# Optimization experiments

Measured on AMD Instinct MI355X. Metric: run time of the kernel, lower is better.

The kernel has to match this reference:

```python
import jax, jax.numpy as jnp
import numpy as np

N_C = 64
D = 128

def setup_inputs() -> dict:
    key = jax.random.key(0)
    embeddings = jax.random.normal(key, (1024, N_C * D), dtype=jnp.float32)
    return {"embeddings": embeddings}

def reference(embeddings) -> jnp.ndarray:
    two_b, _ = embeddings.shape
    B = two_b // 2
    # (2, B, n_c, d), softmax over last dim
    q = jax.nn.softmax(embeddings.reshape(2, B, N_C, D), axis=-1)
    q_a, q_b = q[0], q[1]  # (B, n_c, d)

    self_sim_loss = -(q_a * q_b).sum() / (B * N_C)

    q_a2 = q_a * q_a
    q_b2 = q_b * q_b
    # Faithful to the repeat/repeat_interleave + bmm: block (i, j) of the
    # (n_c^2, d, d) product equals q2[:, j].T @ q2[:, i]  -> einsum over batch.
    prod_a = jnp.einsum('bjc,bid->ijcd', q_a2, q_a2)  # (n_c, n_c, d, d)
    prod_b = jnp.einsum('bjc,bid->ijcd', q_b2, q_b2)

    # mask out diagonal cluster pairs i == j (done before sqrt in original;
    # entries are strictly positive so masking after sqrt is identical)
    offdiag = (~jnp.eye(N_C, dtype=bool))[:, :, None, None]  # (n_c, n_c, 1, 1)

    raw_a = jnp.where(offdiag, jnp.sqrt(prod_a), 0.0).sum()
    raw_b = jnp.where(offdiag, jnp.sqrt(prod_b), 0.0).sum()

    scale = (N_C * N_C - N_C) * (B ** 0.5)
    cluster_loss = -(raw_a / scale + raw_b / scale) / 2
    return self_sim_loss + cluster_loss
```

## Files before the change

kernel.cpp:

```cpp
#include <hip/hip_runtime.h>
#include <cstdint>
#include <cstddef>

#define NCLUS 64
#define DIM   128
#define BATCH 512
#define QCOLS 8192
#define NPAIR 2016
#define TSTRB (QCOLS * BATCH)
#define FP8SCALE 256.0f

typedef float f32x16 __attribute__((ext_vector_type(16)));
typedef int   i32x4  __attribute__((ext_vector_type(4)));
typedef int   i32x8  __attribute__((ext_vector_type(8)));


__device__ __forceinline__ void ld_lds16(const void* g, void* l) {
  __builtin_amdgcn_global_load_lds(
      (__attribute__((address_space(1))) void*)g,
      (__attribute__((address_space(3))) void*)l, 16, 0, 0);
}

#define VM4_BAR() asm volatile("s_waitcnt vmcnt(4)\n\ts_barrier" ::: "memory")
#define VM0_BAR() asm volatile("s_waitcnt vmcnt(0)\n\ts_barrier" ::: "memory")

__global__ __launch_bounds__(512) void softmax_q2_kernel(
    const float* __restrict__ emb, uint8_t* __restrict__ q2t,
    float* __restrict__ dotPart) {
  __shared__ uint32_t T32[2 * 64 * 33];
  __shared__ float red[8];
  const int c  = blockIdx.y;
  const int bq = blockIdx.x;
  const int tid = threadIdx.x;
  const int w = tid >> 6, lane = tid & 63;
  const int sub = lane >> 5;
  const int col = lane & 31;

  float4 qa = {0.f, 0.f, 0.f, 0.f};
  float dot = 0.f;

#pragma unroll
  for (int k = 0; k < 8; ++k) {
    const int t  = k & 1;
    const int bl = w * 8 + (k >> 1) * 2 + sub;
    const int b  = bq * 64 + bl;
    const float4 v = *(const float4*)(emb +
        ((size_t)(t * BATCH + b) * QCOLS + (size_t)c * DIM + col * 4));

    float mx = fmaxf(fmaxf(v.x, v.y), fmaxf(v.z, v.w));
#pragma unroll
    for (int off = 1; off < 32; off <<= 1) mx = fmaxf(mx, __shfl_xor(mx, off));
    float e0 = __expf(v.x - mx), e1 = __expf(v.y - mx);
    float e2 = __expf(v.z - mx), e3 = __expf(v.w - mx);
    float s = (e0 + e1) + (e2 + e3);
#pragma unroll
    for (int off = 1; off < 32; off <<= 1) s += __shfl_xor(s, off);
    const float inv = 1.0f / s;
    const float q0 = e0 * inv, q1 = e1 * inv, q2 = e2 * inv, q3 = e3 * inv;

    if (t == 0) { qa.x = q0; qa.y = q1; qa.z = q2; qa.w = q3; }
    else        { dot += qa.x * q0 + qa.y * q1 + qa.z * q2 + qa.w * q3; }

    int pk = __builtin_amdgcn_cvt_pk_fp8_f32(q0 * q0 * FP8SCALE,
                                             q1 * q1 * FP8SCALE, 0, false);
    pk = __builtin_amdgcn_cvt_pk_fp8_f32(q2 * q2 * FP8SCALE,
                                         q3 * q3 * FP8SCALE, pk, true);
    T32[(t * 64 + bl) * 33 + col] = (uint32_t)pk;
  }
  __syncthreads();

#pragma unroll
  for (int it = 0; it < 2; ++it) {
    int ch = it * 512 + tid;
    int t = ch >> 9, d = (ch >> 2) & 127, b16 = ch & 3;
    const int dq = d >> 2, sh = (d & 3) * 8;
    uint32_t w0 = 0, w1 = 0, w2 = 0, w3 = 0;
#pragma unroll
    for (int r = 0; r < 4; ++r) {
      w0 |= ((T32[(t * 64 + b16 * 16 +  0 + r) * 33 + dq] >> sh) & 0xFFu) << (8 * r);
      w1 |= ((T32[(t * 64 + b16 * 16 +  4 + r) * 33 + dq] >> sh) & 0xFFu) << (8 * r);
      w2 |= ((T32[(t * 64 + b16 * 16 +  8 + r) * 33 + dq] >> sh) & 0xFFu) << (8 * r);
      w3 |= ((T32[(t * 64 + b16 * 16 + 12 + r) * 33 + dq] >> sh) & 0xFFu) << (8 * r);
    }
    size_t off = (size_t)t * TSTRB + (size_t)(c * DIM + d) * BATCH +
                 (size_t)bq * 64 + b16 * 16;
    uint4 o; o.x = w0; o.y = w1; o.z = w2; o.w = w3;
    *(uint4*)(q2t + off) = o;
  }

#pragma unroll
  for (int off = 1; off < 64; off <<= 1) dot += __shfl_xor(dot, off);
  if (lane == 0) red[w] = dot;
  __syncthreads();
  if (tid == 0) {
    float dt = 0.f;
#pragma unroll
    for (int i = 0; i < 8; ++i) dt += red[i];
    dotPart[blockIdx.y * 8 + blockIdx.x] = dt;
  }
}

__global__ __launch_bounds__(256) void gram_sqrt_kernel(
    const uint8_t* __restrict__ q2t, float* __restrict__ Spart) {
  __shared__ uint8_t L[3 * 16384 + 16];

  int sidx = ((int)blockIdx.x & 7) * 252 + ((int)blockIdx.x >> 3);
  int q = sidx, gi = 0;
  while (q >= 64 * gi + 28) { q -= 64 * gi + 28; ++gi; }
  int I, J;
  if (q < 64 * gi) {
    int gj = q >> 6, r = q & 63;
    I = gi * 8 + (r >> 3);
    J = gj * 8 + (r & 7);
  } else {
    int dq = q - 64 * gi;
    int il = 1;
    while (il * (il + 1) / 2 <= dq) ++il;
    I = gi * 8 + il;
    J = gi * 8 + (dq - il * (il - 1) / 2);
  }

  const uint8_t* baseA = q2t + (size_t)J * (DIM * BATCH);
  const uint8_t* baseB = q2t + (size_t)I * (DIM * BATCH);

  const int tid  = threadIdx.x;
  const int lane = tid & 63, w = tid >> 6;
  const int wm = w & 1, wn = w >> 1;

  const int t0 = tid, t1 = 256 + tid;
  const int r0s = t0 >> 2, r1s = t1 >> 2;
  const int rot0 = (r0s + (r0s >> 2)) & 3;
  const int rot1 = (r1s + (r1s >> 2)) & 3;
  const int c0s = ((t0 & 3) - rot0) & 3;
  const int c1s = ((t1 & 3) - rot1) & 3;
  const size_t g0 = (size_t)r0s * BATCH + c0s * 16;
  const size_t g1 = (size_t)r1s * BATCH + c1s * 16;
  uint8_t* Lb = L;
  const int ldsw = w * 1024;

  const int h = lane >> 5, r31 = lane & 31;
  const int rot = (r31 + (r31 >> 2)) & 3;
  const int ro1 = ((2 * h + rot) & 3) * 16;
  const int ro2 = ((2 * h + 1 + rot) & 3) * 16;
  const int ArowO = (wm * 64 + r31) * 64;
  const int BrowO = 8192 + (wn * 64 + r31) * 64;

  f32x16 acc[2][2];
#pragma unroll
  for (int i = 0; i < 2; ++i)
#pragma unroll
    for (int j = 0; j < 2; ++j) acc[i][j] = (f32x16)(0.f);

  float S0 = 0.f, S1 = 0.f;

#define CHOFF64(i) ((size_t)((i) >> 3) * TSTRB + (size_t)((i) & 7) * 64)
#define STAGE(bufb, ck) do {                                       \
    ld_lds16(baseA + (ck) + g0, Lb + (bufb) + ldsw);               \
    ld_lds16(baseA + (ck) + g1, Lb + (bufb) + 4096 + ldsw);        \
    ld_lds16(baseB + (ck) + g0, Lb + (bufb) + 8192 + ldsw);        \
    ld_lds16(baseB + (ck) + g1, Lb + (bufb) + 12288 + ldsw);       \
  } while (0)
#define MFMA(a, b, c) __builtin_amdgcn_mfma_scale_f32_32x32x64_f8f6f4(        \
    (a), (b), (c), 0, 0, 0, 0x7F7F7F7F, 0, 0x7F7F7F7F)

  STAGE(0, CHOFF64(0));
  STAGE(16384, CHOFF64(1));

#pragma unroll
  for (int m = 0; m < 16; ++m) {
    if (m < 15) VM4_BAR(); else VM0_BAR();

    if (m < 14) STAGE(((m + 2) % 3) * 16384, CHOFF64(m + 2));

    const int be = (m % 3) * 16384;
    i32x4 alo[2], ahi[2], blo[2], bhi[2];
#pragma unroll
    for (int g = 0; g < 2; ++g) {
      alo[g] = *(const i32x4*)(Lb + be + ArowO + g * 2048 + ro1);
      ahi[g] = *(const i32x4*)(Lb + be + ArowO + g * 2048 + ro2);
      blo[g] = *(const i32x4*)(Lb + be + BrowO + g * 2048 + ro1);
      bhi[g] = *(const i32x4*)(Lb + be + BrowO + g * 2048 + ro2);
    }
    i32x8 af[2], bf[2];
#pragma unroll
    for (int g = 0; g < 2; ++g) {
      af[g] = (i32x8){alo[g].x, alo[g].y, alo[g].z, alo[g].w,
                      ahi[g].x, ahi[g].y, ahi[g].z, ahi[g].w};
      bf[g] = (i32x8){blo[g].x, blo[g].y, blo[g].z, blo[g].w,
                      bhi[g].x, bhi[g].y, bhi[g].z, bhi[g].w};
    }
    __builtin_amdgcn_s_setprio(1);
#pragma unroll
    for (int i = 0; i < 2; ++i)
#pragma unroll
      for (int j = 0; j < 2; ++j)
        acc[i][j] = MFMA(af[i], bf[j], acc[i][j]);
    __builtin_amdgcn_s_setprio(0);

    if (m == 7) {
#pragma unroll
      for (int i = 0; i < 2; ++i)
#pragma unroll
        for (int j = 0; j < 2; ++j) {
#pragma unroll
          for (int e = 0; e < 16; ++e) S0 += sqrtf(acc[i][j][e]);
          acc[i][j] = (f32x16)(0.f);
        }
    }
  }

#pragma unroll
  for (int i = 0; i < 2; ++i)
#pragma unroll
    for (int j = 0; j < 2; ++j)
#pragma unroll
      for (int e = 0; e < 16; ++e) S1 += sqrtf(acc[i][j][e]);

  float local = (S0 + S1) * (1.0f / 256.0f);
#pragma unroll
  for (int off = 1; off < 64; off <<= 1) local += __shfl_xor(local, off);
  float* fred = (float*)(L + 3 * 16384);
  if (lane == 0) fred[w] = local;
  __syncthreads();
  if (tid == 0) Spart[blockIdx.x] = fred[0] + fred[1] + fred[2] + fred[3];
}

__global__ __launch_bounds__(256) void finalize_kernel(
    const float* __restrict__ P, float* __restrict__ out) {
  __shared__ float rd[8];
  const int tid = threadIdx.x;
  float d = 0.f, s = 0.f;
  for (int i = tid; i < 512; i += 256) d += P[i];
  for (int i = tid; i < NPAIR; i += 256) s += P[512 + i];
#pragma unroll
  for (int off = 1; off < 64; off <<= 1) { d += __shfl_xor(d, off); s += __shfl_xor(s, off); }
  const int w = tid >> 6;
  if ((tid & 63) == 0) { rd[w] = d; rd[4 + w] = s; }
  __syncthreads();
  if (tid == 0) {
    float dt = rd[0] + rd[1] + rd[2] + rd[3];
    float st = rd[4] + rd[5] + rd[6] + rd[7];
    out[0] = -dt / 32768.0f - st / (4032.0f * 22.62741699796952f);
  }
}

extern "C" void kernel_launch(void* const* d_in, const int* in_sizes, int n_in,
                              void* d_out, int out_size, void* d_ws, size_t ws_size,
                              hipStream_t stream) {
  const float* emb = (const float*)d_in[0];
  float* out = (float*)d_out;
  float* P = (float*)d_ws;
  uint8_t* q2t = (uint8_t*)d_ws + 16384;

  softmax_q2_kernel<<<dim3(8, 64), 512, 0, stream>>>(emb, q2t, P);
  gram_sqrt_kernel<<<dim3(NPAIR), 256, 0, stream>>>(q2t, P + 512);
  finalize_kernel<<<1, 256, 0, stream>>>(P, out);
}
```

Baseline: 126.6 us.

## Tile gram kernel over 256x256 cluster-pair super-tiles with 512-thread blocks

Replaces the per-cluster-pair gram kernel (2016 blocks, 128x128 tiles) with a super-tile kernel in which each 512-thread block computes a 256x256 product covering two clusters by two clusters, giving 528 blocks over the lower triangle. Each loaded tile is reused across more MFMAs, which cuts global and LDS traffic per flop. On diagonal super-tiles only the warps holding the strictly off-diagonal cluster pair do MFMAs, so some warps idle there. The softmax kernel also drops to 256 threads per block, with each thread doing twice as many rows.

```diff
diff --git a/kernel.cpp b/kernel.cpp
--- a/kernel.cpp
+++ b/kernel.cpp
@@ -6,7 +6,7 @@
 #define DIM   128
 #define BATCH 512
 #define QCOLS 8192
-#define NPAIR 2016
+#define NSUPER 528
 #define TSTRB (QCOLS * BATCH)
 #define FP8SCALE 256.0f
 
@@ -24,11 +24,11 @@
 #define VM4_BAR() asm volatile("s_waitcnt vmcnt(4)\n\ts_barrier" ::: "memory")
 #define VM0_BAR() asm volatile("s_waitcnt vmcnt(0)\n\ts_barrier" ::: "memory")
 
-__global__ __launch_bounds__(512) void softmax_q2_kernel(
+__global__ __launch_bounds__(256) void softmax_q2_kernel(
     const float* __restrict__ emb, uint8_t* __restrict__ q2t,
     float* __restrict__ dotPart) {
   __shared__ uint32_t T32[2 * 64 * 33];
-  __shared__ float red[8];
+  __shared__ float red[4];
   const int c  = blockIdx.y;
   const int bq = blockIdx.x;
   const int tid = threadIdx.x;
@@ -40,9 +40,9 @@
   float dot = 0.f;
 
 #pragma unroll
-  for (int k = 0; k < 8; ++k) {
+  for (int k = 0; k < 16; ++k) {
     const int t  = k & 1;
-    const int bl = w * 8 + (k >> 1) * 2 + sub;
+    const int bl = w * 16 + (k >> 1) * 2 + sub;
     const int b  = bq * 64 + bl;
     const float4 v = *(const float4*)(emb +
         ((size_t)(t * BATCH + b) * QCOLS + (size_t)c * DIM + col * 4));
@@ -70,8 +70,8 @@
   __syncthreads();
 
 #pragma unroll
-  for (int it = 0; it < 2; ++it) {
-    int ch = it * 512 + tid;
+  for (int it = 0; it < 4; ++it) {
+    int ch = it * 256 + tid;
     int t = ch >> 9, d = (ch >> 2) & 127, b16 = ch & 3;
     const int dq = d >> 2, sh = (d & 3) * 8;
     uint32_t w0 = 0, w1 = 0, w2 = 0, w3 = 0;
@@ -92,49 +92,30 @@
   for (int off = 1; off < 64; off <<= 1) dot += __shfl_xor(dot, off);
   if (lane == 0) red[w] = dot;
   __syncthreads();
-  if (tid == 0) {
-    float dt = 0.f;
-#pragma unroll
-    for (int i = 0; i < 8; ++i) dt += red[i];
-    dotPart[blockIdx.y * 8 + blockIdx.x] = dt;
-  }
-}
-
-__global__ __launch_bounds__(256) void gram_sqrt_kernel(
+  if (tid == 0) dotPart[blockIdx.y * 8 + blockIdx.x] = red[0] + red[1] + red[2] + red[3];
+}
+
+__global__ __launch_bounds__(512, 2) void gram_super_kernel(
     const uint8_t* __restrict__ q2t, float* __restrict__ Spart) {
-  __shared__ uint8_t L[3 * 16384 + 16];
-
-  int sidx = ((int)blockIdx.x & 7) * 252 + ((int)blockIdx.x >> 3);
-  int q = sidx, gi = 0;
-  while (q >= 64 * gi + 28) { q -= 64 * gi + 28; ++gi; }
-  int I, J;
-  if (q < 64 * gi) {
-    int gj = q >> 6, r = q & 63;
-    I = gi * 8 + (r >> 3);
-    J = gj * 8 + (r & 7);
-  } else {
-    int dq = q - 64 * gi;
-    int il = 1;
-    while (il * (il + 1) / 2 <= dq) ++il;
-    I = gi * 8 + il;
-    J = gi * 8 + (dq - il * (il - 1) / 2);
-  }
-
-  const uint8_t* baseA = q2t + (size_t)J * (DIM * BATCH);
-  const uint8_t* baseB = q2t + (size_t)I * (DIM * BATCH);
+  __shared__ uint8_t L[3 * 32768 + 32];
+
+  int sidx = ((int)blockIdx.x & 7) * 66 + ((int)blockIdx.x >> 3);
+  int gi = 0;
+  while ((gi + 1) * (gi + 2) / 2 <= sidx) ++gi;
+  int gj = sidx - gi * (gi + 1) / 2;
+  const bool diag = (gi == gj);
+
+  const uint8_t* baseA = q2t + (size_t)gj * (256 * BATCH);
+  const uint8_t* baseB = q2t + (size_t)gi * (256 * BATCH);
 
   const int tid  = threadIdx.x;
   const int lane = tid & 63, w = tid >> 6;
   const int wm = w & 1, wn = w >> 1;
 
-  const int t0 = tid, t1 = 256 + tid;
-  const int r0s = t0 >> 2, r1s = t1 >> 2;
-  const int rot0 = (r0s + (r0s >> 2)) & 3;
-  const int rot1 = (r1s + (r1s >> 2)) & 3;
-  const int c0s = ((t0 & 3) - rot0) & 3;
-  const int c1s = ((t1 & 3) - rot1) & 3;
-  const size_t g0 = (size_t)r0s * BATCH + c0s * 16;
-  const size_t g1 = (size_t)r1s * BATCH + c1s * 16;
+  const int rs = tid >> 2;
+  const int rot_s = (rs + (rs >> 2)) & 3;
+  const int cs = ((tid & 3) - rot_s) & 3;
+  const size_t gsrc = (size_t)rs * BATCH + cs * 16;
   uint8_t* Lb = L;
   const int ldsw = w * 1024;
 
@@ -142,87 +123,100 @@
   const int rot = (r31 + (r31 >> 2)) & 3;
   const int ro1 = ((2 * h + rot) & 3) * 16;
   const int ro2 = ((2 * h + 1 + rot) & 3) * 16;
-  const int ArowO = (wm * 64 + r31) * 64;
-  const int BrowO = 8192 + (wn * 64 + r31) * 64;
-
-  f32x16 acc[2][2];
-#pragma unroll
-  for (int i = 0; i < 2; ++i)
+  const int ArO = (wm * 128 + r31) * 64;
+  const int BrO = 16384 + (wn * 64 + r31) * 64;
+
+  const bool take = !diag || (wm == 0 && wn >= 2);
+
+  f32x16 acc[4][2];
+#pragma unroll
+  for (int i = 0; i < 4; ++i)
 #pragma unroll
     for (int j = 0; j < 2; ++j) acc[i][j] = (f32x16)(0.f);
 
   float S0 = 0.f, S1 = 0.f;
 
 #define CHOFF64(i) ((size_t)((i) >> 3) * TSTRB + (size_t)((i) & 7) * 64)
-#define STAGE(bufb, ck) do {                                       \
-    ld_lds16(baseA + (ck) + g0, Lb + (bufb) + ldsw);               \
-    ld_lds16(baseA + (ck) + g1, Lb + (bufb) + 4096 + ldsw);        \
-    ld_lds16(baseB + (ck) + g0, Lb + (bufb) + 8192 + ldsw);        \
-    ld_lds16(baseB + (ck) + g1, Lb + (bufb) + 12288 + ldsw);       \
+#define STAGE(bufb, ck) do {                                           \
+    ld_lds16(baseA + (ck) + gsrc,         Lb + (bufb) + ldsw);         \
+    ld_lds16(baseA + (ck) + gsrc + 65536, Lb + (bufb) + 8192 + ldsw);  \
+    ld_lds16(baseB + (ck) + gsrc,         Lb + (bufb) + 16384 + ldsw); \
+    ld_lds16(baseB + (ck) + gsrc + 65536, Lb + (bufb) + 24576 + ldsw); \
   } while (0)
 #define MFMA(a, b, c) __builtin_amdgcn_mfma_scale_f32_32x32x64_f8f6f4(        \
     (a), (b), (c), 0, 0, 0, 0x7F7F7F7F, 0, 0x7F7F7F7F)
+#define CAT8(lo, hi) __builtin_shufflevector((lo), (hi), 0, 1, 2, 3, 4, 5, 6, 7)
 
   STAGE(0, CHOFF64(0));
-  STAGE(16384, CHOFF64(1));
+  STAGE(32768, CHOFF64(1));
 
 #pragma unroll
   for (int m = 0; m < 16; ++m) {
     if (m < 15) VM4_BAR(); else VM0_BAR();
 
-    if (m < 14) STAGE(((m + 2) % 3) * 16384, CHOFF64(m + 2));
-
-    const int be = (m % 3) * 16384;
-    i32x4 alo[2], ahi[2], blo[2], bhi[2];
-#pragma unroll
-    for (int g = 0; g < 2; ++g) {
-      alo[g] = *(const i32x4*)(Lb + be + ArowO + g * 2048 + ro1);
-      ahi[g] = *(const i32x4*)(Lb + be + ArowO + g * 2048 + ro2);
-      blo[g] = *(const i32x4*)(Lb + be + BrowO + g * 2048 + ro1);
-      bhi[g] = *(const i32x4*)(Lb + be + BrowO + g * 2048 + ro2);
+    if (m < 14) STAGE(((m + 2) % 3) * 32768, CHOFF64(m + 2));
+
+    if (take) {
+      const int be = (m % 3) * 32768;
+      i32x8 af[4], bf[2];
+#pragma unroll
+      for (int mi = 0; mi < 4; ++mi) {
+        i32x4 lo = *(const i32x4*)(Lb + be + ArO + mi * 2048 + ro1);
+        i32x4 hi = *(const i32x4*)(Lb + be + ArO + mi * 2048 + ro2);
+        af[mi] = CAT8(lo, hi);
+      }
+#pragma unroll
+      for (int nj = 0; nj < 2; ++nj) {
+        i32x4 lo = *(const i32x4*)(Lb + be + BrO + nj * 2048 + ro1);
+        i32x4 hi = *(const i32x4*)(Lb + be + BrO + nj * 2048 + ro2);
+        bf[nj] = CAT8(lo, hi);
+      }
+      __builtin_amdgcn_s_setprio(1);
+#pragma unroll
+      for (int mi = 0; mi < 4; ++mi)
+#pragma unroll
+        for (int nj = 0; nj < 2; ++nj)
+          acc[mi][nj] = MFMA(af[mi], bf[nj], acc[mi][nj]);
+      __builtin_amdgcn_s_setprio(0);
     }
-    i32x8 af[2], bf[2];
-#pragma unroll
-    for (int g = 0; g < 2; ++g) {
-      af[g] = (i32x8){alo[g].x, alo[g].y, alo[g].z, alo[g].w,
-                      ahi[g].x, ahi[g].y, ahi[g].z, ahi[g].w};
-      bf[g] = (i32x8){blo[g].x, blo[g].y, blo[g].z, blo[g].w,
-                      bhi[g].x, bhi[g].y, bhi[g].z, bhi[g].w};
+
+    if (m == 7) {
+      if (take) {
+#pragma unroll
+        for (int i = 0; i < 4; ++i)
+#pragma unroll
+          for (int j = 0; j < 2; ++j)
+#pragma unroll
+            for (int e = 0; e < 16; ++e) S0 += sqrtf(acc[i][j][e]);
+      }
+#pragma unroll
+      for (int i = 0; i < 4; ++i)
+#pragma unroll
+        for (int j = 0; j < 2; ++j) acc[i][j] = (f32x16)(0.f);
     }
-    __builtin_amdgcn_s_setprio(1);
-#pragma unroll
-    for (int i = 0; i < 2; ++i)
+  }
+
+  if (take) {
+#pragma unroll
+    for (int i = 0; i < 4; ++i)
 #pragma unroll
       for (int j = 0; j < 2; ++j)
-        acc[i][j] = MFMA(af[i], bf[j], acc[i][j]);
-    __builtin_amdgcn_s_setprio(0);
-
-    if (m == 7) {
-#pragma unroll
-      for (int i = 0; i < 2; ++i)
-#pragma unroll
-        for (int j = 0; j < 2; ++j) {
-#pragma unroll
-          for (int e = 0; e < 16; ++e) S0 += sqrtf(acc[i][j][e]);
-          acc[i][j] = (f32x16)(0.f);
-        }
-    }
-  }
-
-#pragma unroll
-  for (int i = 0; i < 2; ++i)
-#pragma unroll
-    for (int j = 0; j < 2; ++j)
-#pragma unroll
-      for (int e = 0; e < 16; ++e) S1 += sqrtf(acc[i][j][e]);
+#pragma unroll
+        for (int e = 0; e < 16; ++e) S1 += sqrtf(acc[i][j][e]);
+  }
 
   float local = (S0 + S1) * (1.0f / 256.0f);
 #pragma unroll
   for (int off = 1; off < 64; off <<= 1) local += __shfl_xor(local, off);
-  float* fred = (float*)(L + 3 * 16384);
+  float* fred = (float*)(L + 3 * 32768);
   if (lane == 0) fred[w] = local;
   __syncthreads();
-  if (tid == 0) Spart[blockIdx.x] = fred[0] + fred[1] + fred[2] + fred[3];
+  if (tid == 0) {
+    float t = 0.f;
+#pragma unroll
+    for (int i = 0; i < 8; ++i) t += fred[i];
+    Spart[blockIdx.x] = t;
+  }
 }
 
 __global__ __launch_bounds__(256) void finalize_kernel(
@@ -231,7 +225,7 @@
   const int tid = threadIdx.x;
   float d = 0.f, s = 0.f;
   for (int i = tid; i < 512; i += 256) d += P[i];
-  for (int i = tid; i < NPAIR; i += 256) s += P[512 + i];
+  for (int i = tid; i < NSUPER; i += 256) s += P[512 + i];
 #pragma unroll
   for (int off = 1; off < 64; off <<= 1) { d += __shfl_xor(d, off); s += __shfl_xor(s, off); }
   const int w = tid >> 6;
@@ -252,7 +246,7 @@
   float* P = (float*)d_ws;
   uint8_t* q2t = (uint8_t*)d_ws + 16384;
 
-  softmax_q2_kernel<<<dim3(8, 64), 512, 0, stream>>>(emb, q2t, P);
-  gram_sqrt_kernel<<<dim3(NPAIR), 256, 0, stream>>>(q2t, P + 512);
+  softmax_q2_kernel<<<dim3(8, 64), 256, 0, stream>>>(emb, q2t, P);
+  gram_super_kernel<<<dim3(NSUPER), 512, 0, stream>>>(q2t, P + 512);
   finalize_kernel<<<1, 256, 0, stream>>>(P, out);
 }
```

After: 156.3 us. 1.23x slower.
